# Performance work log

Hardware: AMD Instinct MI355X
Metric: run time of the kernel (lower is better)

The kernel has to match this reference:

```python
import jax, jax.numpy as jnp
import numpy as np

# lct_fk config (matches init_kwargs)
BIN_LEN = 0.01
WALL_SIZE = 2.0
C_LIGHT = 3.0e8


def _safe_sqrt(v):
    # sqrt(relu(v)) with a well-defined (zero) subgradient at v<=0
    pos = v > 0
    return jnp.where(pos, jnp.sqrt(jnp.where(pos, v, 1.0)), 0.0)


def _trilinear_zero(vol, pz, py, px):
    # vol: (D,H,W) complex64; pz/py/px: (D2,H2,W2) float pixel coords
    # Trilinear sampling with zeros padding (== F.grid_sample align_corners=False)
    D, H, W = vol.shape
    z0f = jnp.floor(pz); y0f = jnp.floor(py); x0f = jnp.floor(px)
    dz = pz - z0f; dy = py - y0f; dx = px - x0f
    z0 = z0f.astype(jnp.int32); y0 = y0f.astype(jnp.int32); x0 = x0f.astype(jnp.int32)
    out = jnp.zeros(pz.shape, vol.dtype)
    for iz, wz in ((z0, 1.0 - dz), (z0 + 1, dz)):
        for iy, wy in ((y0, 1.0 - dy), (y0 + 1, dy)):
            for ix, wx in ((x0, 1.0 - dx), (x0 + 1, dx)):
                valid = (iz >= 0) & (iz < D) & (iy >= 0) & (iy < H) & (ix >= 0) & (ix < W)
                v = vol[jnp.clip(iz, 0, D - 1), jnp.clip(iy, 0, H - 1), jnp.clip(ix, 0, W - 1)]
                w = jnp.where(valid, wz * wy * wx, 0.0)
                out = out + w * v
    return out


def setup_inputs() -> dict:
    key = jax.random.key(0)
    feture = jax.random.uniform(key, (1, 2, 128, 128, 128), dtype=jnp.float32)
    return {"feture_bxdxtxhxw": feture}


def reference(feture_bxdxtxhxw):
    b, d, T, H, W = feture_bxdxtxhxw.shape
    M, N = T, H  # temprol_grid (== crop), sptial_grid; tbes=0, tens=crop -> no temporal pad
    width = WALL_SIZE / 2.0
    trange = M * BIN_LEN  # crop * c * (bin_len/c)

    # z-weighting: (z/(M-1))^2, then sqrt(relu(.))
    gridz = (jnp.arange(M, dtype=jnp.float32) / (M - 1)).reshape(1, M, 1, 1)
    data = feture_bxdxtxhxw.reshape(b * d, T, H, W) * (gridz ** 2)
    data = _safe_sqrt(jax.nn.relu(data))

    # zero-pad to (2T,2H,2W), FFT, fftshift (roll by half == fftshift for even sizes)
    datapad = jnp.pad(data, ((0, 0), (0, M), (0, N), (0, N)))
    fre = jnp.fft.fftshift(jnp.fft.fftn(datapad, axes=(-3, -2, -1)), axes=(-3, -2, -1))

    # Stolt (f-k) warped coordinates, normalized to [-1,1]
    zdim = (jnp.arange(2 * M, dtype=jnp.float32) - M) / M
    xdim = (jnp.arange(2 * N, dtype=jnp.float32) - N) / N
    gz = zdim[:, None, None]            # varies along axis 0
    gy = xdim[None, :, None]            # varies along axis 1
    gx = xdim[None, None, :]            # varies along axis 2
    fk = (N * trange / (M * width * 4.0)) ** 2
    gznew = jnp.sqrt(fk * (gx ** 2 + gy ** 2) + gz ** 2)  # (2M,2N,2N)
    gznew = jnp.broadcast_to(gznew, (2 * M, 2 * N, 2 * N))

    # unnormalize (align_corners=False): pix = ((c+1)*size - 1)/2
    px = ((jnp.broadcast_to(gx, gznew.shape) + 1.0) * (2 * N) - 1.0) * 0.5
    py = ((jnp.broadcast_to(gy, gznew.shape) + 1.0) * (2 * N) - 1.0) * 0.5
    pz = ((gznew + 1.0) * (2 * M) - 1.0) * 0.5

    samp = jax.vmap(lambda v: _trilinear_zero(v, pz, py, px))(fre)

    # zero negative/zero frequencies along z, then Stolt Jacobian scaling
    z0pos = M + 1  # first index where zdim > 0
    zmask = (jnp.arange(2 * M) >= z0pos)[None, :, None, None]
    samp = samp * zmask
    samp = samp * (jnp.abs(gz) / (gznew + 1e-8))[None]

    samp = jnp.fft.fftshift(samp, axes=(-3, -2, -1))  # ifftshift == fftshift (even dims)
    vol = jnp.fft.ifftn(samp, axes=(-3, -2, -1))
    out = vol[:, :M, :N, :N].real
    return out.reshape(b, d, M, N, N)
```

## Files before the change

kernel.cpp:

```cpp
#include <hip/hip_runtime.h>

static constexpr size_t VS   = 8388608;
static constexpr int    ZSTR = 65536;
static constexpr int    YSTR = 256;
static constexpr size_t VSB  = 4194304;
static constexpr int    BZS  = 32768;
static constexpr int    BYS  = 128;
static constexpr int    LSTR = 261;

typedef float vf2 __attribute__((ext_vector_type(2)));

__device__ __forceinline__ vf2 cmul(vf2 a, vf2 b){
    vf2 asw; asw.x = -a.y; asw.y = a.x;
    return a*b.x + asw*b.y;
}

constexpr int BREV(int k){ return ((k&1)<<3)|((k&2)<<1)|((k&4)>>1)|((k&8)>>3); }

__device__ __forceinline__ void bf(vf2& a, vf2& b, float c, float s){
    vf2 sum = a + b;
    vf2 dif = a - b;
    vf2 dsw; dsw.x = -dif.y; dsw.y = dif.x;
    b = dif*c + dsw*s;
    a = sum;
}

template<int DIR>
__device__ __forceinline__ void fft16(vf2 r[16]){
    constexpr float D = (float)DIR;
    constexpr float C16[8] = {1.f, 0.92387953f, 0.70710678f, 0.38268343f, 0.f, -0.38268343f, -0.70710678f, -0.92387953f};
    constexpr float S16[8] = {0.f, 0.38268343f, 0.70710678f, 0.92387953f, 1.f, 0.92387953f, 0.70710678f, 0.38268343f};
#pragma unroll
    for (int j = 0; j < 8; ++j) bf(r[j], r[j+8], C16[j], D*S16[j]);
    constexpr float C8[4] = {1.f, 0.70710678f, 0.f, -0.70710678f};
    constexpr float S8[4] = {0.f, 0.70710678f, 1.f, 0.70710678f};
#pragma unroll
    for (int g = 0; g < 16; g += 8)
#pragma unroll
        for (int j = 0; j < 4; ++j) bf(r[g+j], r[g+j+4], C8[j], D*S8[j]);
#pragma unroll
    for (int g = 0; g < 16; g += 4){
        bf(r[g],   r[g+2], 1.f, 0.f);
        bf(r[g+1], r[g+3], 0.f, D);
    }
#pragma unroll
    for (int g = 0; g < 16; g += 2) bf(r[g], r[g+1], 1.f, 0.f);
}

__device__ __forceinline__ void init_tw(vf2* tw, float dir){
    int tid = threadIdx.x;
    float ang = dir * 0.0245436926f * (float)((tid >> 4)*(tid & 15));
    float s, c; __sincosf(ang, &s, &c);
    vf2 w; w.x = c; w.y = s;
    tw[tid] = w;
}

template<int DIR>
__device__ __forceinline__ void mid256s(vf2 r[16], vf2* sh8, const vf2* tw, int t, int l){
    fft16<DIR>(r);
#pragma unroll
    for (int k1 = 1; k1 < 16; ++k1)
        r[BREV(k1)] = cmul(r[BREV(k1)], tw[k1*16 + t]);
    int lr = l & 7;
    bool lo = (l < 8);
    __syncthreads();
    if (lo){
#pragma unroll
        for (int k1 = 0; k1 < 16; ++k1) sh8[lr*LSTR + k1*16 + (t ^ k1)] = r[BREV(k1)];
    }
    __syncthreads();
    if (lo){
#pragma unroll
        for (int n2 = 0; n2 < 16; ++n2) r[n2] = sh8[lr*LSTR + t*16 + (n2 ^ t)];
    }
    __syncthreads();
    if (!lo){
#pragma unroll
        for (int k1 = 0; k1 < 16; ++k1) sh8[lr*LSTR + k1*16 + (t ^ k1)] = r[BREV(k1)];
    }
    __syncthreads();
    if (!lo){
#pragma unroll
        for (int n2 = 0; n2 < 16; ++n2) r[n2] = sh8[lr*LSTR + t*16 + (n2 ^ t)];
    }
    fft16<DIR>(r);
}

template<int DIR>
__device__ __forceinline__ void mid256w(vf2 r[16], vf2* shw, const vf2* tw, int t, int l){
    fft16<DIR>(r);
#pragma unroll
    for (int k1 = 1; k1 < 16; ++k1)
        r[BREV(k1)] = cmul(r[BREV(k1)], tw[k1*16 + t]);
    vf2* base = shw + ((l >> 2)*2 + (l & 1))*LSTR;
    if ((l & 2) == 0){
#pragma unroll
        for (int k1 = 0; k1 < 16; ++k1) base[k1*16 + (t ^ k1)] = r[BREV(k1)];
#pragma unroll
        for (int n2 = 0; n2 < 16; ++n2) r[n2] = base[t*16 + (n2 ^ t)];
    }
    __builtin_amdgcn_sched_barrier(0);
    if ((l & 2) != 0){
#pragma unroll
        for (int k1 = 15; k1 >= 0; --k1) base[k1*16 + (t ^ k1)] = r[BREV(k1)];
#pragma unroll
        for (int n2 = 15; n2 >= 0; --n2) r[n2] = base[t*16 + (n2 ^ t)];
    }
    fft16<DIR>(r);
}

template<int DIR, int NIN, int NOUT>
__device__ __forceinline__ void fft_strided(vf2* g, int S){
    __shared__ vf2 sh8[8*LSTR];
    __shared__ vf2 tw[256];
    int t = threadIdx.x >> 4, l = threadIdx.x & 15;
    vf2 r[16];
    vf2 zero; zero.x = 0.f; zero.y = 0.f;
#pragma unroll
    for (int n1 = 0; n1 < 16; ++n1)
        r[n1] = (n1 < NIN/16) ? g[(size_t)(16*n1 + t)*S + l] : zero;
    init_tw(tw, (float)DIR);
    __syncthreads();
    mid256s<DIR>(r, sh8, tw, t, l);
#pragma unroll
    for (int k2 = 0; k2 < 16; ++k2)
        if (k2 < NOUT/16) g[(size_t)(t + 16*k2)*S + l] = r[BREV(k2)];
}

__global__ void __launch_bounds__(256) k_p1(const float* __restrict__ in, vf2* __restrict__ A){
    __shared__ vf2 sh8[8*LSTR];
    __shared__ vf2 tw[256];
    __shared__ float shin[16*130];
    init_tw(tw, -1.f);
    int th = threadIdx.x, bid = blockIdx.x;
    int yc = bid & 7, z = (bid >> 3) & 127, v = bid >> 10;
    float gz = z * (1.0f/127.0f);
    float g2 = gz*gz;
    const float* src = in + (((size_t)(v*128 + z))*128 + yc*16)*128;
    for (int idx = th; idx < 2048; idx += 256){
        float val = src[idx] * g2;
        shin[(idx >> 7)*130 + (idx & 127)] = val > 0.f ? sqrtf(val) : 0.f;
    }
    __syncthreads();
    int t = th >> 4, l = th & 15;
    vf2 r[16];
    vf2 zero; zero.x = 0.f; zero.y = 0.f;
#pragma unroll
    for (int n1 = 0; n1 < 16; ++n1){
        r[n1] = zero;
        if (n1 < 8) r[n1].x = shin[l*130 + 16*n1 + t];
    }
    mid256s<-1>(r, sh8, tw, t, l);
    int lr = l & 7;
    vf2* dst = A + (size_t)v*VS + (size_t)z*ZSTR + (size_t)(yc*16)*YSTR;
#pragma unroll
    for (int half = 0; half < 2; ++half){
        __syncthreads();
        if ((l >> 3) == half){
#pragma unroll
            for (int k2 = 0; k2 < 16; ++k2) sh8[lr*LSTR + t + 16*k2] = r[BREV(k2)];
        }
        __syncthreads();
        vf2* d2 = dst + half*8*YSTR;
        for (int idx = th; idx < 2048; idx += 256){
            int line = idx >> 8, k = idx & 255;
            vf2 a = sh8[line*LSTR + k];
            vf2 p = sh8[line*LSTR + ((k - 1) & 255)];
            if (k == 128) p = zero;
            d2[idx] = (a + p)*0.5f;
        }
    }
}

__global__ void __launch_bounds__(256) k_p2z(vf2* __restrict__ A){
    int bid = blockIdx.x;
    int xb = bid & 15, y = (bid >> 4) & 127, v = bid >> 11;
    fft_strided<-1,128,128>(A + (size_t)v*VS + (size_t)y*YSTR + xb*16, ZSTR);
}

__global__ void __launch_bounds__(256) k_p3y(vf2* __restrict__ A){
    __shared__ vf2 sh8[8*LSTR];
    __shared__ vf2 tw[256];
    __shared__ vf2 shW[64];
    int bid = blockIdx.x;
    int xb = bid & 15, z = (bid >> 4) & 127, v = bid >> 11;
    vf2* g = A + (size_t)v*VS + (size_t)z*ZSTR + xb*16;
    int t = threadIdx.x >> 4, l = threadIdx.x & 15;
    vf2 r[16];
    vf2 zero; zero.x = 0.f; zero.y = 0.f;
#pragma unroll
    for (int n1 = 0; n1 < 16; ++n1)
        r[n1] = (n1 < 8) ? g[(size_t)(16*n1 + t)*YSTR + l] : zero;

    vf2 part = ((r[0]+r[1]) + (r[2]+r[3])) + ((r[4]+r[5]) + (r[6]+r[7]));
    part = part * ((t & 1) ? -1.f : 1.f);
    part.x += __shfl_xor(part.x, 16);
    part.y += __shfl_xor(part.y, 16);
    part.x += __shfl_xor(part.x, 32);
    part.y += __shfl_xor(part.y, 32);
    if ((t & 3) == 0) shW[(t >> 2)*16 + l] = part;

#pragma unroll
    for (int n1 = 0; n1 < 8; ++n1){
        float sn, cn; __sincosf(0.0245436926f * (float)(16*n1 + t), &sn, &cn);
        vf2 c; c.x = 0.5f*(1.f + cn); c.y = 0.5f*sn;
        r[n1] = cmul(r[n1], c);
    }

    init_tw(tw, -1.f);
    __syncthreads();
    mid256s<-1>(r, sh8, tw, t, l);

    if (t == 0){
        vf2 S = (shW[l] + shW[16 + l]) + (shW[32 + l] + shW[48 + l]);
        r[BREV(8)] = S * 0.5f;
    }
#pragma unroll
    for (int k2 = 0; k2 < 16; ++k2)
        g[(size_t)(t + 16*k2)*YSTR + l] = r[BREV(k2)];
}

__global__ void __launch_bounds__(256) k_p45(const vf2* __restrict__ A, vf2* __restrict__ B){
    __shared__ vf2 sh8[8*LSTR];
    __shared__ vf2 tw[256];
    init_tw(tw, 1.f);
    int tid = threadIdx.x, bid = blockIdx.x;
    int yc = bid & 15, zn = (bid >> 4) & 127, v = bid >> 11;
    const vf2* Av = A + (size_t)v*VS;
    int t = tid & 15, l = tid >> 4;
    int yn = yc*16 + l;
    float gy = (yn < 128 ? yn : yn - 256) * (1.0f/128.0f);
    float gz = zn * (1.0f/128.0f);
    float c2 = 0.1024f*gy*gy + gz*gz;
    unsigned rowoff = (unsigned)yn*YSTR;
    vf2 r[16];
#pragma unroll
    for (int n1 = 0; n1 < 16; ++n1){
        int xn = 16*n1 + t;
        float gx = (xn < 128 ? xn : xn - 256) * (1.0f/128.0f);
        float s2 = c2 + 0.1024f*gx*gx;
        float rs = __builtin_amdgcn_rsqf(s2 + 1e-12f);
        float gznew = s2 * rs;
        float pz = gznew*128.0f + 127.5f;
        int zi = (int)pz;
        float dz = pz - (float)zi;
        int zp0 = zi - 128;
        float wf = gz * rs;
        float w0 = (((unsigned)zp0     < 128u) ? (1.0f - dz) : 0.f) * wf;
        float w1 = (((unsigned)(zp0+1) < 128u) ? dz : 0.f) * wf;
        vf2 v0 = Av[(size_t)((unsigned)(zp0 & 127) * ZSTR) + rowoff + xn];
        vf2 v1 = Av[(size_t)((unsigned)((zp0 + 1) & 127) * ZSTR) + rowoff + xn];
        r[n1] = v0*w0 + v1*w1;
    }
    __syncthreads();
    mid256w<1>(r, sh8, tw, t, l);
    vf2* dst = B + (size_t)v*VSB + (size_t)zn*BZS + (size_t)yn*BYS;
#pragma unroll
    for (int k2 = 0; k2 < 8; ++k2)
        dst[t + 16*k2] = r[BREV(k2)];
}

__global__ void __launch_bounds__(256) k_p6(vf2* __restrict__ B){
    int bid = blockIdx.x;
    int xb = bid & 7, zn = (bid >> 3) & 127, v = bid >> 10;
    fft_strided<1,256,128>(B + (size_t)v*VSB + (size_t)zn*BZS + xb*16, BYS);
}

__global__ void __launch_bounds__(256) k_p7(const vf2* __restrict__ B, float* __restrict__ out){
    __shared__ vf2 sh8[8*LSTR];
    __shared__ vf2 tw[256];
    int bid = blockIdx.x;
    int xb = bid & 7, y = (bid >> 3) & 127, v = bid >> 10;
    const vf2* g = B + (size_t)v*VSB + (size_t)y*BYS + xb*16;
    int t = threadIdx.x >> 4, l = threadIdx.x & 15;
    vf2 r[16];
    vf2 zero; zero.x = 0.f; zero.y = 0.f;
#pragma unroll
    for (int n1 = 0; n1 < 16; ++n1)
        r[n1] = (n1 < 8) ? g[(size_t)(16*n1 + t)*BZS + l] : zero;
    init_tw(tw, 1.f);
    __syncthreads();
    mid256s<1>(r, sh8, tw, t, l);
    const float sc = 1.0f/16777216.0f;
    float* dst = out + ((size_t)(v*128)*128 + y)*128 + xb*16 + l;
#pragma unroll
    for (int k2 = 0; k2 < 8; ++k2)
        dst[(size_t)(t + 16*k2)*16384] = r[BREV(k2)].x * sc;
}

extern "C" void kernel_launch(void* const* d_in, const int* in_sizes, int n_in,
                              void* d_out, int out_size, void* d_ws, size_t ws_size,
                              hipStream_t stream){
    const float* in = (const float*)d_in[0];
    float* out = (float*)d_out;
    vf2* A = (vf2*)d_ws;
    vf2* B = A + 2*VS;
    k_p1 <<< 2048, 256, 0, stream>>>(in, A);
    k_p2z<<< 4096, 256, 0, stream>>>(A);
    k_p3y<<< 4096, 256, 0, stream>>>(A);
    k_p45<<< 4096, 256, 0, stream>>>(A, B);
    k_p6 <<< 2048, 256, 0, stream>>>(B);
    k_p7 <<< 2048, 256, 0, stream>>>(B, out);
}
```

Before: 200.0 us.

## Fold x-axis interpolation averaging into pre-twiddled FFT input in first pass

The first-pass kernel no longer stages input through shared memory, and it no longer does a post-FFT shared-memory pass to average neighboring frequency bins. Instead it multiplies the input by a (1+e^{iθ})/2 factor before the FFT, which is equivalent to averaging adjacent output bins. The one bin that wraps is fixed up with a wave-shuffle alternating-sign reduction. It also switches to a wave-local transpose that computes twiddles on the fly with sincos, removing the shared twiddle table and several block syncs. This trades shared-memory traffic and barriers for extra transcendental math and recurrence rounding error in the twiddles.

```diff
diff --git a/kernel.cpp b/kernel.cpp
--- a/kernel.cpp
+++ b/kernel.cpp
@@ -86,26 +86,45 @@
     fft16<DIR>(r);
 }
 
+__device__ __forceinline__ void wave_transpose(vf2 r[16], vf2* shw, int t, int l){
+    vf2* base = shw + ((l >> 2)*2 + (l & 1))*LSTR;
+    if ((l & 2) == 0){
+#pragma unroll
+        for (int k1 = 0; k1 < 16; ++k1) base[k1*16 + (t ^ k1)] = r[BREV(k1)];
+#pragma unroll
+        for (int n2 = 0; n2 < 16; ++n2) r[n2] = base[t*16 + (n2 ^ t)];
+    }
+    __builtin_amdgcn_sched_barrier(0);
+    if ((l & 2) != 0){
+#pragma unroll
+        for (int k1 = 15; k1 >= 0; --k1) base[k1*16 + (t ^ k1)] = r[BREV(k1)];
+#pragma unroll
+        for (int n2 = 15; n2 >= 0; --n2) r[n2] = base[t*16 + (n2 ^ t)];
+    }
+}
+
 template<int DIR>
 __device__ __forceinline__ void mid256w(vf2 r[16], vf2* shw, const vf2* tw, int t, int l){
     fft16<DIR>(r);
 #pragma unroll
     for (int k1 = 1; k1 < 16; ++k1)
         r[BREV(k1)] = cmul(r[BREV(k1)], tw[k1*16 + t]);
-    vf2* base = shw + ((l >> 2)*2 + (l & 1))*LSTR;
-    if ((l & 2) == 0){
-#pragma unroll
-        for (int k1 = 0; k1 < 16; ++k1) base[k1*16 + (t ^ k1)] = r[BREV(k1)];
-#pragma unroll
-        for (int n2 = 0; n2 < 16; ++n2) r[n2] = base[t*16 + (n2 ^ t)];
-    }
-    __builtin_amdgcn_sched_barrier(0);
-    if ((l & 2) != 0){
-#pragma unroll
-        for (int k1 = 15; k1 >= 0; --k1) base[k1*16 + (t ^ k1)] = r[BREV(k1)];
-#pragma unroll
-        for (int n2 = 15; n2 >= 0; --n2) r[n2] = base[t*16 + (n2 ^ t)];
-    }
+    wave_transpose(r, shw, t, l);
+    fft16<DIR>(r);
+}
+
+template<int DIR>
+__device__ __forceinline__ void mid256wr(vf2 r[16], vf2* shw, int t, int l){
+    fft16<DIR>(r);
+    float sn, cn; __sincosf((float)DIR * 0.0245436926f * (float)t, &sn, &cn);
+    vf2 w; w.x = cn; w.y = sn;
+    vf2 wk = w;
+#pragma unroll
+    for (int k1 = 1; k1 < 16; ++k1){
+        r[BREV(k1)] = cmul(r[BREV(k1)], wk);
+        wk = cmul(wk, w);
+    }
+    wave_transpose(r, shw, t, l);
     fft16<DIR>(r);
 }
 
@@ -129,47 +148,42 @@
 
 __global__ void __launch_bounds__(256) k_p1(const float* __restrict__ in, vf2* __restrict__ A){
     __shared__ vf2 sh8[8*LSTR];
-    __shared__ vf2 tw[256];
-    __shared__ float shin[16*130];
-    init_tw(tw, -1.f);
-    int th = threadIdx.x, bid = blockIdx.x;
+    int tid = threadIdx.x, bid = blockIdx.x;
     int yc = bid & 7, z = (bid >> 3) & 127, v = bid >> 10;
+    int t = tid & 15, l = tid >> 4;
     float gz = z * (1.0f/127.0f);
     float g2 = gz*gz;
-    const float* src = in + (((size_t)(v*128 + z))*128 + yc*16)*128;
-    for (int idx = th; idx < 2048; idx += 256){
-        float val = src[idx] * g2;
-        shin[(idx >> 7)*130 + (idx & 127)] = val > 0.f ? sqrtf(val) : 0.f;
-    }
-    __syncthreads();
-    int t = th >> 4, l = th & 15;
+    const float* src = in + (((size_t)(v*128 + z))*128 + yc*16 + l)*128;
+    float val[8];
+#pragma unroll
+    for (int n1 = 0; n1 < 8; ++n1) val[n1] = src[16*n1 + t];
+#pragma unroll
+    for (int n1 = 0; n1 < 8; ++n1){
+        float x = val[n1] * g2;
+        val[n1] = x > 0.f ? sqrtf(x) : 0.f;
+    }
+    float part = ((val[0]+val[1]) + (val[2]+val[3])) + ((val[4]+val[5]) + (val[6]+val[7]));
+    part = (t & 1) ? -part : part;
+    part += __shfl_xor(part, 1);
+    part += __shfl_xor(part, 2);
+    part += __shfl_xor(part, 4);
+    part += __shfl_xor(part, 8);
     vf2 r[16];
     vf2 zero; zero.x = 0.f; zero.y = 0.f;
 #pragma unroll
-    for (int n1 = 0; n1 < 16; ++n1){
-        r[n1] = zero;
-        if (n1 < 8) r[n1].x = shin[l*130 + 16*n1 + t];
-    }
-    mid256s<-1>(r, sh8, tw, t, l);
-    int lr = l & 7;
-    vf2* dst = A + (size_t)v*VS + (size_t)z*ZSTR + (size_t)(yc*16)*YSTR;
-#pragma unroll
-    for (int half = 0; half < 2; ++half){
-        __syncthreads();
-        if ((l >> 3) == half){
-#pragma unroll
-            for (int k2 = 0; k2 < 16; ++k2) sh8[lr*LSTR + t + 16*k2] = r[BREV(k2)];
-        }
-        __syncthreads();
-        vf2* d2 = dst + half*8*YSTR;
-        for (int idx = th; idx < 2048; idx += 256){
-            int line = idx >> 8, k = idx & 255;
-            vf2 a = sh8[line*LSTR + k];
-            vf2 p = sh8[line*LSTR + ((k - 1) & 255)];
-            if (k == 128) p = zero;
-            d2[idx] = (a + p)*0.5f;
-        }
-    }
+    for (int n1 = 8; n1 < 16; ++n1) r[n1] = zero;
+#pragma unroll
+    for (int n1 = 0; n1 < 8; ++n1){
+        float sn, cn; __sincosf(0.0245436926f * (float)(16*n1 + t), &sn, &cn);
+        r[n1].x = val[n1] * 0.5f * (1.f + cn);
+        r[n1].y = val[n1] * 0.5f * sn;
+    }
+    mid256wr<-1>(r, sh8, t, l);
+    if (t == 0){ r[1].x = part*0.5f; r[1].y = 0.f; }
+    vf2* dst = A + (size_t)v*VS + (size_t)z*ZSTR + (size_t)(yc*16 + l)*YSTR;
+#pragma unroll
+    for (int k2 = 0; k2 < 16; ++k2)
+        dst[t + 16*k2] = r[BREV(k2)];
 }
 
 __global__ void __launch_bounds__(256) k_p2z(vf2* __restrict__ A){
```

Measured after the change: 195.6 us. 1.02x faster.
